# Kernel tuning notes

Hardware: AMD Instinct MI355X
Metric: run time of the kernel (lower is better)

## Reference

```python
import jax, jax.numpy as jnp
import numpy as np

B, S, D, H = 2, 2048, 1024, 16
DK = D // H
EPS = 1e-5


def setup_inputs() -> dict:
    key = jax.random.key(0)
    ks = jax.random.split(key, 6)
    std = (2.0 / (D + D)) ** 0.5
    return {
        "x": jax.random.normal(ks[0], (B, S, D), dtype=jnp.float32),
        "W_Q": jax.random.normal(ks[1], (D, D), dtype=jnp.float32) * std,
        "W_K": jax.random.normal(ks[2], (D, D), dtype=jnp.float32) * std,
        "W_V": jax.random.normal(ks[3], (D, D), dtype=jnp.float32) * std,
        "W_O": jax.random.normal(ks[4], (D, D), dtype=jnp.float32) * std,
        "gain": jnp.ones((D,), dtype=jnp.float32),
        "positions": jnp.arange(S, dtype=jnp.int64 if jax.config.jax_enable_x64 else jnp.int32),
        "theta": 10000,
        "max_seq_len": 2048,
    }


def rmsnorm(x, gain):
    xf = x.astype(jnp.float32)
    rms = jnp.sqrt(jnp.mean(xf * xf, axis=-1, keepdims=True) + EPS)
    return ((xf / rms) * gain).astype(x.dtype)


def apply_rope(x, sin, cos):
    # x: [..., seq, dk]; sin/cos: [seq, dk//2] broadcast over leading dims
    x_even = x[..., 0::2]
    x_odd = x[..., 1::2]
    r_even = x_even * cos - x_odd * sin
    r_odd = x_odd * cos + x_even * sin
    return jnp.stack([r_even, r_odd], axis=-1).reshape(x.shape)


def reference(x, W_Q, W_K, W_V, W_O, gain, positions, theta, max_seq_len):
    seq_len = x.shape[-2]
    Q = jnp.einsum('od,bsd->bso', W_Q, x)
    K = jnp.einsum('od,bsd->bso', W_K, x)
    V = jnp.einsum('od,bsd->bso', W_V, x)
    # RMSNorm over full d_model BEFORE head split (as in original)
    Q = rmsnorm(Q, gain)
    K = rmsnorm(K, gain)
    # split heads: [b, h, s, dk]
    Q = Q.reshape(*Q.shape[:-1], H, DK).swapaxes(-3, -2)
    K = K.reshape(*K.shape[:-1], H, DK).swapaxes(-3, -2)
    V = V.reshape(*V.shape[:-1], H, DK).swapaxes(-3, -2)
    # RoPE tables
    exponents = 2.0 * jnp.arange(DK // 2, dtype=jnp.float32) / DK
    inv_freq = 1.0 / (jnp.float32(theta) ** exponents)
    angles = positions.astype(jnp.float32)[:, None] * inv_freq[None, :]  # [S, DK//2]
    sin, cos = jnp.sin(angles), jnp.cos(angles)
    Q = apply_rope(Q, sin, cos)
    K = apply_rope(K, sin, cos)
    # causal attention
    scores = jnp.einsum('bhqd,bhkd->bhqk', Q, K) / jnp.sqrt(jnp.float32(DK))
    causal = jnp.tril(jnp.ones((seq_len, seq_len), dtype=bool))
    scores = jnp.where(causal, scores, -jnp.inf)
    attn = jax.nn.softmax(scores, axis=-1)
    out = jnp.einsum('bhqk,bhkd->bhqd', attn, V)
    out = out.swapaxes(-3, -2).reshape(*x.shape[:-1], D)
    return jnp.einsum('of,bsf->bso', W_O, out)
```

## Files before the change

kernel.cpp:

```cpp
#include <hip/hip_runtime.h>
#include <hip/hip_bf16.h>

typedef __attribute__((ext_vector_type(8))) __bf16 bf16x8;
typedef __attribute__((ext_vector_type(4))) __bf16 bf16x4;
typedef __attribute__((ext_vector_type(4))) float  f32x4;
typedef __attribute__((ext_vector_type(4))) short  s16x4;

#define S_LEN 2048
#define D_DIM 1024
#define NH    16
#define GK    1024
#define GN    1024

__device__ __forceinline__ float fast_exp2(float x) {
#if __has_builtin(__builtin_amdgcn_exp2f)
  return __builtin_amdgcn_exp2f(x);
#else
  return exp2f(x);
#endif
}

__device__ __forceinline__ f32x4 mfma16(bf16x4 a, bf16x4 b, f32x4 c) {
#if __has_builtin(__builtin_amdgcn_mfma_f32_16x16x16_bf16)
  return __builtin_amdgcn_mfma_f32_16x16x16_bf16(a, b, c, 0, 0, 0);
#else
  return __builtin_amdgcn_mfma_f32_16x16x16bf16_1k(
      __builtin_bit_cast(s16x4, a), __builtin_bit_cast(s16x4, b), c, 0, 0, 0);
#endif
}

__device__ __forceinline__ void gld_lds16(const void* g, void* l) {
  __builtin_amdgcn_global_load_lds(
      (const __attribute__((address_space(1))) unsigned int*)g,
      (__attribute__((address_space(3))) unsigned int*)l, 16, 0, 0);
}

__global__ __launch_bounds__(256) void cast_all(
    const float* __restrict__ x,  const float* __restrict__ wq, const float* __restrict__ wk,
    const float* __restrict__ wv, const float* __restrict__ wo,
    __bf16* __restrict__ xb, __bf16* __restrict__ wqb, __bf16* __restrict__ wkb,
    __bf16* __restrict__ wvb, __bf16* __restrict__ wob)
{
  const int NTOT = 2 << 20;
  for (int i = blockIdx.x * 256 + threadIdx.x; i < NTOT; i += 1024 * 256) {
    const float* s; __bf16* d; int off;
    if (i < (1 << 20)) { s = x; d = xb; off = i; }
    else {
      const int j = i - (1 << 20);
      const int r = j >> 18; off = j & ((1 << 18) - 1);
      s = (r == 0) ? wq : (r == 1) ? wk : (r == 2) ? wv : wo;
      d = (r == 0) ? wqb : (r == 1) ? wkb : (r == 2) ? wvb : wob;
    }
    float4 v = ((const float4*)s)[off];
    bf16x4 o = { (__bf16)v.x, (__bf16)v.y, (__bf16)v.z, (__bf16)v.w };
    ((bf16x4*)d)[off] = o;
  }
}

__global__ __launch_bounds__(256, 3) void gemm_qkv(
    const __bf16* __restrict__ A,
    const __bf16* __restrict__ W0, const __bf16* __restrict__ W1, const __bf16* __restrict__ W2,
    __bf16* __restrict__ C0, __bf16* __restrict__ C1, __bf16* __restrict__ VtOut)
{
  const int bid = blockIdx.x;
  const int e = bid & 7, mg = e >> 1, ng = e & 1;
  const int q = bid >> 3;
  const int mt = mg * 8 + (q & 7);
  const int nt = ng * 12 + (q >> 3);
  const int mode = nt >> 3;
  const int m0 = mt * 128;
  const int n0 = (nt & 7) * 128;
  const __bf16* Wm = (mode == 0) ? W0 : (mode == 1) ? W1 : W2;

  __shared__ __align__(16) __bf16 As[128 * 64];
  __shared__ __align__(16) __bf16 Bs[128 * 64];

  const int tid  = threadIdx.x;
  const int lane = tid & 63;
  const int w    = tid >> 6;
  const int wr   = w >> 1, wc = w & 1;
  const int lm   = lane & 15, qd = lane >> 4;

  const __bf16* ap[4]; int loA[4];
  #pragma unroll
  for (int j = 0; j < 4; j++) {
    const int c = tid + 256 * j;
    const int r = c >> 3, cpos = c & 7;
    ap[j] = A + (size_t)(m0 + r) * GK + (cpos ^ (r & 7)) * 8;
    loA[j] = c * 8;
  }
  const __bf16* bp[4]; int loB[4];
  #pragma unroll
  for (int j = 0; j < 4; j++) {
    const int c = tid + 256 * j;
    const int r = c >> 3, cpos = c & 7;
    bp[j] = Wm + (size_t)(n0 + r) * GK + (cpos ^ (r & 7)) * 8;
    loB[j] = c * 8;
  }

  const int sw = lm & 7;

  f32x4 zero = {0.f, 0.f, 0.f, 0.f};
  f32x4 acc[4][4];
  #pragma unroll
  for (int i = 0; i < 4; i++)
    #pragma unroll
    for (int j = 0; j < 4; j++) acc[i][j] = zero;

  for (int k0 = 0; k0 < GK; k0 += 64) {
    #pragma unroll
    for (int j = 0; j < 4; j++) gld_lds16(ap[j] + k0, &As[loA[j]]);
    #pragma unroll
    for (int j = 0; j < 4; j++) gld_lds16(bp[j] + k0, &Bs[loB[j]]);
    __syncthreads();
    #pragma unroll
    for (int half = 0; half < 2; half++) {
      const int cph = ((qd + 4 * half) ^ sw) * 8;
      bf16x8 af[4], bfv[4];
      #pragma unroll
      for (int i = 0; i < 4; i++) af[i]  = *(const bf16x8*)&As[(wr * 64 + i * 16 + lm) * 64 + cph];
      #pragma unroll
      for (int j = 0; j < 4; j++) bfv[j] = *(const bf16x8*)&Bs[(wc * 64 + j * 16 + lm) * 64 + cph];
      #pragma unroll
      for (int i = 0; i < 4; i++)
        #pragma unroll
        for (int j = 0; j < 4; j++)
          acc[i][j] = __builtin_amdgcn_mfma_f32_16x16x32_bf16(af[i], bfv[j], acc[i][j], 0, 0, 0);
    }
    __syncthreads();
  }

  if (mode < 2) {
    __bf16* C = (mode == 0) ? C0 : C1;
    #pragma unroll
    for (int i = 0; i < 4; i++) {
      const int row = m0 + wr * 64 + i * 16 + qd * 4;
      #pragma unroll
      for (int j = 0; j < 4; j++) {
        const int col = n0 + wc * 64 + j * 16 + lm;
        #pragma unroll
        for (int r = 0; r < 4; r++)
          C[(size_t)(row + r) * GN + col] = (__bf16)acc[i][j][r];
      }
    }
  } else {
    #pragma unroll
    for (int i = 0; i < 4; i++) {
      const int row = m0 + wr * 64 + i * 16 + qd * 4;
      const int b = row >> 11, s = row & (S_LEN - 1);
      #pragma unroll
      for (int j = 0; j < 4; j++) {
        const int col = n0 + wc * 64 + j * 16 + lm;
        const int h = col >> 6, d = col & 63;
        bf16x4 o = { (__bf16)acc[i][j][0], (__bf16)acc[i][j][1],
                     (__bf16)acc[i][j][2], (__bf16)acc[i][j][3] };
        *(bf16x4*)(VtOut + (((size_t)(b * NH + h) * 64 + d) * S_LEN + s)) = o;
      }
    }
  }
}

__global__ __launch_bounds__(256, 2) void gemm_out64(
    const __bf16* __restrict__ A, const __bf16* __restrict__ Wm, float* __restrict__ C)
{
  const int bid = blockIdx.x;
  const int e = bid & 7, mg = e >> 1, ng = e & 1;
  const int q = bid >> 3;
  const int m0 = (mg * 16 + (q & 15)) * 64;
  const int n0 = (ng * 4 + (q >> 4)) * 128;

  __shared__ __align__(16) __bf16 As[2][64 * 64];
  __shared__ __align__(16) __bf16 Bs[2][128 * 64];

  const int tid  = threadIdx.x;
  const int lane = tid & 63;
  const int w    = tid >> 6;
  const int wr   = w >> 1, wc = w & 1;
  const int lm   = lane & 15, qd = lane >> 4;

  const __bf16* ap[2]; int loA[2];
  #pragma unroll
  for (int j = 0; j < 2; j++) {
    const int c = tid + 256 * j;
    const int r = c >> 3, cpos = c & 7;
    ap[j] = A + (size_t)(m0 + r) * GK + (cpos ^ (r & 7)) * 8;
    loA[j] = c * 8;
  }
  const __bf16* bp[4]; int loB[4];
  #pragma unroll
  for (int j = 0; j < 4; j++) {
    const int c = tid + 256 * j;
    const int r = c >> 3, cpos = c & 7;
    bp[j] = Wm + (size_t)(n0 + r) * GK + (cpos ^ (r & 7)) * 8;
    loB[j] = c * 8;
  }

  const int sw = lm & 7;

  auto stage = [&](int buf, int k0) {
    #pragma unroll
    for (int j = 0; j < 2; j++) gld_lds16(ap[j] + k0, &As[buf][loA[j]]);
    #pragma unroll
    for (int j = 0; j < 4; j++) gld_lds16(bp[j] + k0, &Bs[buf][loB[j]]);
  };

  f32x4 zero = {0.f, 0.f, 0.f, 0.f};
  f32x4 acc[2][4];
  #pragma unroll
  for (int i = 0; i < 2; i++)
    #pragma unroll
    for (int j = 0; j < 4; j++) acc[i][j] = zero;

  stage(0, 0);

  for (int kt = 0; kt < 16; ++kt) {
    const int cur = kt & 1;
    __syncthreads();
    if (kt < 15) stage(cur ^ 1, (kt + 1) * 64);
    #pragma unroll
    for (int half = 0; half < 2; half++) {
      const int cph = ((qd + 4 * half) ^ sw) * 8;
      bf16x8 af[2], bfv[4];
      #pragma unroll
      for (int i = 0; i < 2; i++) af[i]  = *(const bf16x8*)&As[cur][(wr * 32 + i * 16 + lm) * 64 + cph];
      #pragma unroll
      for (int j = 0; j < 4; j++) bfv[j] = *(const bf16x8*)&Bs[cur][(wc * 64 + j * 16 + lm) * 64 + cph];
      #pragma unroll
      for (int i = 0; i < 2; i++)
        #pragma unroll
        for (int j = 0; j < 4; j++)
          acc[i][j] = __builtin_amdgcn_mfma_f32_16x16x32_bf16(af[i], bfv[j], acc[i][j], 0, 0, 0);
    }
  }

  #pragma unroll
  for (int i = 0; i < 2; i++) {
    const int row = m0 + wr * 32 + i * 16 + qd * 4;
    #pragma unroll
    for (int j = 0; j < 4; j++) {
      const int col = n0 + wc * 64 + j * 16 + lm;
      #pragma unroll
      for (int r = 0; r < 4; r++)
        C[(size_t)(row + r) * GN + col] = acc[i][j][r];
    }
  }
}

__global__ __launch_bounds__(256) void norm_rope(
    const __bf16* __restrict__ Qf, const __bf16* __restrict__ Kf,
    const float* __restrict__ gain, const int* __restrict__ positions,
    const int* __restrict__ theta_p,
    __bf16* __restrict__ Qh, __bf16* __restrict__ Kh)
{
  const int row = blockIdx.x;
  const int s = row & (S_LEN - 1), b = row >> 11;
  const int t = threadIdx.x, d0 = t * 4;

  const bf16x4 qv = *(const bf16x4*)(Qf + (size_t)row * D_DIM + d0);
  const bf16x4 kv = *(const bf16x4*)(Kf + (size_t)row * D_DIM + d0);
  const float q0 = (float)qv[0], q1 = (float)qv[1], q2 = (float)qv[2], q3 = (float)qv[3];
  const float k0 = (float)kv[0], k1 = (float)kv[1], k2 = (float)kv[2], k3 = (float)kv[3];

  float sq = q0 * q0 + q1 * q1 + q2 * q2 + q3 * q3;
  float sk = k0 * k0 + k1 * k1 + k2 * k2 + k3 * k3;
  #pragma unroll
  for (int off = 32; off; off >>= 1) { sq += __shfl_xor(sq, off); sk += __shfl_xor(sk, off); }
  __shared__ float red[8];
  const int lane = t & 63, wv = t >> 6;
  if (lane == 0) { red[wv] = sq; red[4 + wv] = sk; }
  __syncthreads();
  sq = red[0] + red[1] + red[2] + red[3];
  sk = red[4] + red[5] + red[6] + red[7];
  const float SC2 = 0.125f * 1.44269504089f;
  const float invq = rsqrtf(sq * (1.0f / 1024.0f) + 1e-5f) * SC2;
  const float invk = rsqrtf(sk * (1.0f / 1024.0f) + 1e-5f);

  const float4 g = *(const float4*)(gain + d0);
  const float qn0 = q0 * invq * g.x, qn1 = q1 * invq * g.y;
  const float qn2 = q2 * invq * g.z, qn3 = q3 * invq * g.w;
  const float kn0 = k0 * invk * g.x, kn1 = k1 * invk * g.y;
  const float kn2 = k2 * invk * g.z, kn3 = k3 * invk * g.w;

  const float pos = (float)positions[s];
  const float th  = (float)theta_p[0];
  const int idx = d0 & 63, h = d0 >> 6, p0 = idx >> 1;
  const float lg32 = __log2f(th) * (1.0f / 32.0f);
  const float f0 = fast_exp2(-(float)p0 * lg32);
  const float f1 = fast_exp2(-(float)(p0 + 1) * lg32);
  float s0, cc0, s1, cc1;
  __sincosf(pos * f0, &s0, &cc0);
  __sincosf(pos * f1, &s1, &cc1);

  const float qe0 = qn0 * cc0 - qn1 * s0, qo0 = qn1 * cc0 + qn0 * s0;
  const float qe1 = qn2 * cc1 - qn3 * s1, qo1 = qn3 * cc1 + qn2 * s1;
  const float ke0 = kn0 * cc0 - kn1 * s0, ko0 = kn1 * cc0 + kn0 * s0;
  const float ke1 = kn2 * cc1 - kn3 * s1, ko1 = kn3 * cc1 + kn2 * s1;

  const size_t obase = ((size_t)((b * NH + h) * S_LEN + s)) * 64 + idx;
  bf16x4 qo = { (__bf16)qe0, (__bf16)qo0, (__bf16)qe1, (__bf16)qo1 };
  bf16x4 ko = { (__bf16)ke0, (__bf16)ko0, (__bf16)ke1, (__bf16)ko1 };
  *(bf16x4*)(Qh + obase) = qo;
  *(bf16x4*)(Kh + obase) = ko;
}

__global__ __launch_bounds__(256) void attn_fwd(
    const __bf16* __restrict__ Qh, const __bf16* __restrict__ Kh,
    const __bf16* __restrict__ Vt, __bf16* __restrict__ Ob)
{
  const int bid = blockIdx.x;
  const int g   = bid >> 5, gj = g & 7, gs = g >> 3;
  const int qt  = (gs == 0) ? 31 - gj : (gs == 1) ? gj : (gs == 2) ? 23 - gj : 8 + gj;
  const int rr  = bid & 31;
  const int bh  = (rr & 7) * 4 + (rr >> 3);
  const int tid = threadIdx.x, lane = tid & 63, w = tid >> 6;
  const int lm = lane & 15, qd = lane >> 4;

  __shared__ __align__(16) __bf16 smem[8192 + 8192];
  __bf16* Ks = smem;
  __bf16* Vs = smem + 8192;

  const int row0 = qt * 64 + w * 16;
  const int qglob = row0 + lm;
  const size_t qbase = (size_t)bh * S_LEN * 64;
  const bf16x8 aq0 = *(const bf16x8*)(Qh + qbase + (size_t)qglob * 64 + qd * 8);
  const bf16x8 aq1 = *(const bf16x8*)(Qh + qbase + (size_t)qglob * 64 + 32 + qd * 8);

  const __bf16* Kb = Kh + (size_t)bh * S_LEN * 64;
  const __bf16* Vb = Vt + (size_t)bh * 64 * S_LEN;
  const int c0 = tid, c1 = 256 + tid;
  const int kr0 = c0 >> 3, kr1 = c1 >> 3;
  const int kg0 = ((c0 & 7) ^ (kr0 & 7)) * 8;
  const int kg1 = ((c1 & 7) ^ (kr1 & 7)) * 8;
  const int cpA = (qd ^ (lm & 7)) * 8;
  const int cpB = cpA ^ 32;

  auto stage = [&](int buf, int k0) {
    __bf16* Kd = Ks + buf * 4096;
    __bf16* Vd = Vs + buf * 4096;
    gld_lds16(Kb + (size_t)(k0 + kr0) * 64 + kg0, &Kd[c0 * 8]);
    gld_lds16(Kb + (size_t)(k0 + kr1) * 64 + kg1, &Kd[c1 * 8]);
    gld_lds16(Vb + (size_t)kr0 * S_LEN + k0 + kg0, &Vd[c0 * 8]);
    gld_lds16(Vb + (size_t)kr1 * S_LEN + k0 + kg1, &Vd[c1 * 8]);
  };

  f32x4 zero = {0.f, 0.f, 0.f, 0.f};
  f32x4 lacc = zero;
  f32x4 o[4];
  #pragma unroll
  for (int jb = 0; jb < 4; jb++) o[jb] = zero;

  bf16x4 ones4;
  #pragma unroll
  for (int i = 0; i < 4; i++) ones4[i] = (__bf16)1.0f;

  stage(0, 0);

  for (int kt = 0; kt <= qt; ++kt) {
    const int cur = kt & 1;
    __syncthreads();
    if (kt < qt) stage(cur ^ 1, (kt + 1) * 64);

    const __bf16* Kc = Ks + cur * 4096;
    const __bf16* Vc = Vs + cur * 4096;
    const int k0 = kt * 64;
    const bool diag = (kt == qt);

    bf16x4 pfrag[4];
    #pragma unroll
    for (int kb = 0; kb < 4; kb++) {
      const int krow = (kb * 16 + lm) * 64;
      const bf16x8 ak0 = *(const bf16x8*)&Kc[krow + cpA];
      const bf16x8 ak1 = *(const bf16x8*)&Kc[krow + cpB];
      f32x4 sc = zero;
      sc = __builtin_amdgcn_mfma_f32_16x16x32_bf16(ak0, aq0, sc, 0, 0, 0);
      sc = __builtin_amdgcn_mfma_f32_16x16x32_bf16(ak1, aq1, sc, 0, 0, 0);
      float p[4];
      if (diag) {
        const int keyb = k0 + kb * 16 + qd * 4;
        #pragma unroll
        for (int r = 0; r < 4; r++)
          p[r] = (keyb + r <= qglob) ? fast_exp2(sc[r]) : 0.f;
      } else {
        #pragma unroll
        for (int r = 0; r < 4; r++) p[r] = fast_exp2(sc[r]);
      }
      bf16x4 pf = { (__bf16)p[0], (__bf16)p[1], (__bf16)p[2], (__bf16)p[3] };
      pfrag[kb] = pf;
      lacc = mfma16(ones4, pf, lacc);
    }

    #pragma unroll
    for (int jb = 0; jb < 4; jb++) {
      const int vrow = jb * 16 + lm;
      const int rsw = vrow & 7;
      #pragma unroll
      for (int kb = 0; kb < 4; kb++) {
        const int c = 2 * kb + (qd >> 1);
        const bf16x4 av = *(const bf16x4*)&Vc[vrow * 64 + ((c ^ rsw) << 3) + (qd & 1) * 4];
        o[jb] = mfma16(av, pfrag[kb], o[jb]);
      }
    }
  }

  const int b = bh >> 4, h = bh & 15;
  const float inv = 1.0f / lacc[0];
  const size_t base = ((size_t)(b * S_LEN + qglob)) * D_DIM + h * 64 + qd * 4;
  #pragma unroll
  for (int jb = 0; jb < 4; jb++) {
    bf16x4 ov = { (__bf16)(o[jb][0] * inv), (__bf16)(o[jb][1] * inv),
                  (__bf16)(o[jb][2] * inv), (__bf16)(o[jb][3] * inv) };
    *(bf16x4*)(Ob + base + jb * 16) = ov;
  }
}

extern "C" void kernel_launch(void* const* d_in, const int* in_sizes, int n_in,
                              void* d_out, int out_size, void* d_ws, size_t ws_size,
                              hipStream_t stream)
{
  (void)in_sizes; (void)n_in; (void)out_size; (void)ws_size;
  const float* x    = (const float*)d_in[0];
  const float* WQ   = (const float*)d_in[1];
  const float* WK   = (const float*)d_in[2];
  const float* WV   = (const float*)d_in[3];
  const float* WO   = (const float*)d_in[4];
  const float* gain = (const float*)d_in[5];
  const int* positions = (const int*)d_in[6];
  const int* theta     = (const int*)d_in[7];
  float* out = (float*)d_out;

  char* ws = (char*)d_ws;
  const size_t MB = 1024 * 1024;
  __bf16* xb  = (__bf16*)(ws + 0);
  __bf16* WQb = (__bf16*)(ws + 8  * MB);
  __bf16* WKb = (__bf16*)(ws + 10 * MB);
  __bf16* WVb = (__bf16*)(ws + 12 * MB);
  __bf16* WOb = (__bf16*)(ws + 14 * MB);
  __bf16* Qfb = (__bf16*)(ws + 16 * MB);
  __bf16* Kfb = (__bf16*)(ws + 24 * MB);
  __bf16* Vt  = (__bf16*)(ws + 32 * MB);
  __bf16* Qh  = (__bf16*)(ws + 40 * MB);
  __bf16* Kh  = (__bf16*)(ws + 48 * MB);
  __bf16* Ob  = (__bf16*)(ws + 56 * MB);

  cast_all<<<1024, 256, 0, stream>>>(x, WQ, WK, WV, WO, xb, WQb, WKb, WVb, WOb);
  gemm_qkv<<<768, 256, 0, stream>>>(xb, WQb, WKb, WVb, Qfb, Kfb, Vt);
  norm_rope<<<4096, 256, 0, stream>>>(Qfb, Kfb, gain, positions, theta, Qh, Kh);
  attn_fwd<<<1024, 256, 0, stream>>>(Qh, Kh, Vt, Ob);
  gemm_out64<<<512, 256, 0, stream>>>(Ob, WOb, out);
}
```

Measured before the change: 180.6 us.

## Process 128-query tiles per attention block with two 16-row fragments per wave

The attention kernel now handles 128 query rows per block, each wave computing two 16-row query fragments against every staged K/V tile, and launches half as many blocks. Each K/V tile loaded into shared memory is reused for twice as many queries, which cuts global K/V traffic and staging overhead per query. In exchange each block does more diagonal work: waves whose rows end before a tile skip it but still join its barriers, so load is less even. The extra accumulators also raise register pressure, and only 512 blocks may underfill the GPU.

```diff
diff --git a/kernel.cpp b/kernel.cpp
--- a/kernel.cpp
+++ b/kernel.cpp
@@ -308,8 +308,9 @@
     const __bf16* __restrict__ Vt, __bf16* __restrict__ Ob)
 {
   const int bid = blockIdx.x;
-  const int g   = bid >> 5, gj = g & 7, gs = g >> 3;
-  const int qt  = (gs == 0) ? 31 - gj : (gs == 1) ? gj : (gs == 2) ? 23 - gj : 8 + gj;
+  const int g   = bid >> 5;
+  const int gj = g & 7, gs = g >> 3;
+  const int qt  = gs ? gj : 15 - gj;
   const int rr  = bid & 31;
   const int bh  = (rr & 7) * 4 + (rr >> 3);
   const int tid = threadIdx.x, lane = tid & 63, w = tid >> 6;
@@ -319,11 +320,13 @@
   __bf16* Ks = smem;
   __bf16* Vs = smem + 8192;
 
-  const int row0 = qt * 64 + w * 16;
-  const int qglob = row0 + lm;
+  const int qA = qt * 128 + w * 32 + lm;
+  const int qB = qA + 16;
   const size_t qbase = (size_t)bh * S_LEN * 64;
-  const bf16x8 aq0 = *(const bf16x8*)(Qh + qbase + (size_t)qglob * 64 + qd * 8);
-  const bf16x8 aq1 = *(const bf16x8*)(Qh + qbase + (size_t)qglob * 64 + 32 + qd * 8);
+  const bf16x8 aqA0 = *(const bf16x8*)(Qh + qbase + (size_t)qA * 64 + qd * 8);
+  const bf16x8 aqA1 = *(const bf16x8*)(Qh + qbase + (size_t)qA * 64 + 32 + qd * 8);
+  const bf16x8 aqB0 = *(const bf16x8*)(Qh + qbase + (size_t)qB * 64 + qd * 8);
+  const bf16x8 aqB1 = *(const bf16x8*)(Qh + qbase + (size_t)qB * 64 + 32 + qd * 8);
 
   const __bf16* Kb = Kh + (size_t)bh * S_LEN * 64;
   const __bf16* Vb = Vt + (size_t)bh * 64 * S_LEN;
@@ -344,49 +347,60 @@
   };
 
   f32x4 zero = {0.f, 0.f, 0.f, 0.f};
-  f32x4 lacc = zero;
-  f32x4 o[4];
-  #pragma unroll
-  for (int jb = 0; jb < 4; jb++) o[jb] = zero;
+  f32x4 laccA = zero, laccB = zero;
+  f32x4 oA[4], oB[4];
+  #pragma unroll
+  for (int jb = 0; jb < 4; jb++) { oA[jb] = zero; oB[jb] = zero; }
 
   bf16x4 ones4;
   #pragma unroll
   for (int i = 0; i < 4; i++) ones4[i] = (__bf16)1.0f;
 
+  const int NT = 2 * qt + 2;
+  const int wq0 = qt * 128 + w * 32;
+
   stage(0, 0);
 
-  for (int kt = 0; kt <= qt; ++kt) {
+  for (int kt = 0; kt < NT; ++kt) {
     const int cur = kt & 1;
     __syncthreads();
-    if (kt < qt) stage(cur ^ 1, (kt + 1) * 64);
+    if (kt < NT - 1) stage(cur ^ 1, (kt + 1) * 64);
+
+    const int k0 = kt * 64;
+    if (k0 > wq0 + 31) continue;
 
     const __bf16* Kc = Ks + cur * 4096;
     const __bf16* Vc = Vs + cur * 4096;
-    const int k0 = kt * 64;
-    const bool diag = (kt == qt);
-
-    bf16x4 pfrag[4];
+    const bool needMask = (k0 + 63 > wq0);
+
+    bf16x4 pfA[4], pfB[4];
     #pragma unroll
     for (int kb = 0; kb < 4; kb++) {
       const int krow = (kb * 16 + lm) * 64;
       const bf16x8 ak0 = *(const bf16x8*)&Kc[krow + cpA];
       const bf16x8 ak1 = *(const bf16x8*)&Kc[krow + cpB];
-      f32x4 sc = zero;
-      sc = __builtin_amdgcn_mfma_f32_16x16x32_bf16(ak0, aq0, sc, 0, 0, 0);
-      sc = __builtin_amdgcn_mfma_f32_16x16x32_bf16(ak1, aq1, sc, 0, 0, 0);
-      float p[4];
-      if (diag) {
+      f32x4 scA = zero, scB = zero;
+      scA = __builtin_amdgcn_mfma_f32_16x16x32_bf16(ak0, aqA0, scA, 0, 0, 0);
+      scB = __builtin_amdgcn_mfma_f32_16x16x32_bf16(ak0, aqB0, scB, 0, 0, 0);
+      scA = __builtin_amdgcn_mfma_f32_16x16x32_bf16(ak1, aqA1, scA, 0, 0, 0);
+      scB = __builtin_amdgcn_mfma_f32_16x16x32_bf16(ak1, aqB1, scB, 0, 0, 0);
+      float pA[4], pB[4];
+      if (needMask) {
         const int keyb = k0 + kb * 16 + qd * 4;
         #pragma unroll
-        for (int r = 0; r < 4; r++)
-          p[r] = (keyb + r <= qglob) ? fast_exp2(sc[r]) : 0.f;
+        for (int r = 0; r < 4; r++) {
+          pA[r] = (keyb + r <= qA) ? fast_exp2(scA[r]) : 0.f;
+          pB[r] = (keyb + r <= qB) ? fast_exp2(scB[r]) : 0.f;
+        }
       } else {
         #pragma unroll
-        for (int r = 0; r < 4; r++) p[r] = fast_exp2(sc[r]);
+        for (int r = 0; r < 4; r++) { pA[r] = fast_exp2(scA[r]); pB[r] = fast_exp2(scB[r]); }
       }
-      bf16x4 pf = { (__bf16)p[0], (__bf16)p[1], (__bf16)p[2], (__bf16)p[3] };
-      pfrag[kb] = pf;
-      lacc = mfma16(ones4, pf, lacc);
+      bf16x4 fA = { (__bf16)pA[0], (__bf16)pA[1], (__bf16)pA[2], (__bf16)pA[3] };
+      bf16x4 fB = { (__bf16)pB[0], (__bf16)pB[1], (__bf16)pB[2], (__bf16)pB[3] };
+      pfA[kb] = fA; pfB[kb] = fB;
+      laccA = mfma16(ones4, fA, laccA);
+      laccB = mfma16(ones4, fB, laccB);
     }
 
     #pragma unroll
@@ -397,19 +411,25 @@
       for (int kb = 0; kb < 4; kb++) {
         const int c = 2 * kb + (qd >> 1);
         const bf16x4 av = *(const bf16x4*)&Vc[vrow * 64 + ((c ^ rsw) << 3) + (qd & 1) * 4];
-        o[jb] = mfma16(av, pfrag[kb], o[jb]);
+        oA[jb] = mfma16(av, pfA[kb], oA[jb]);
+        oB[jb] = mfma16(av, pfB[kb], oB[jb]);
       }
     }
   }
 
   const int b = bh >> 4, h = bh & 15;
-  const float inv = 1.0f / lacc[0];
-  const size_t base = ((size_t)(b * S_LEN + qglob)) * D_DIM + h * 64 + qd * 4;
+  const float invA = 1.0f / laccA[0];
+  const float invB = 1.0f / laccB[0];
+  const size_t baseA = ((size_t)(b * S_LEN + qA)) * D_DIM + h * 64 + qd * 4;
+  const size_t baseB = baseA + (size_t)16 * D_DIM;
   #pragma unroll
   for (int jb = 0; jb < 4; jb++) {
-    bf16x4 ov = { (__bf16)(o[jb][0] * inv), (__bf16)(o[jb][1] * inv),
-                  (__bf16)(o[jb][2] * inv), (__bf16)(o[jb][3] * inv) };
-    *(bf16x4*)(Ob + base + jb * 16) = ov;
+    bf16x4 ovA = { (__bf16)(oA[jb][0] * invA), (__bf16)(oA[jb][1] * invA),
+                   (__bf16)(oA[jb][2] * invA), (__bf16)(oA[jb][3] * invA) };
+    bf16x4 ovB = { (__bf16)(oB[jb][0] * invB), (__bf16)(oB[jb][1] * invB),
+                   (__bf16)(oB[jb][2] * invB), (__bf16)(oB[jb][3] * invB) };
+    *(bf16x4*)(Ob + baseA + jb * 16) = ovA;
+    *(bf16x4*)(Ob + baseB + jb * 16) = ovB;
   }
 }
 
@@ -445,6 +465,6 @@
   cast_all<<<1024, 256, 0, stream>>>(x, WQ, WK, WV, WO, xb, WQb, WKb, WVb, WOb);
   gemm_qkv<<<768, 256, 0, stream>>>(xb, WQb, WKb, WVb, Qfb, Kfb, Vt);
   norm_rope<<<4096, 256, 0, stream>>>(Qfb, Kfb, gain, positions, theta, Qh, Kh);
-  attn_fwd<<<1024, 256, 0, stream>>>(Qh, Kh, Vt, Ob);
+  attn_fwd<<<512, 256, 0, stream>>>(Qh, Kh, Vt, Ob);
   gemm_out64<<<512, 256, 0, stream>>>(Ob, WOb, out);
 }
```

Measured after the change: 189.3 us. 4.8% more time.
